# Kernel tuning notes

Measured on AMD Instinct MI355X. Metric: run time of the kernel, lower is better.

## Reference

```python
import jax, jax.numpy as jnp
import numpy as np

N_NODES = 50000
N_EDGES = 800000
D_IN = 64
D_OUT = 64


def setup_inputs() -> dict:
    key = jax.random.key(0)
    k1, k2, k3, k4 = jax.random.split(key, 4)
    x = jax.random.normal(k1, (N_NODES, D_IN), dtype=jnp.float32)
    src = jax.random.randint(k2, (N_EDGES,), 0, N_NODES, dtype=jnp.int64)
    dst = jax.random.randint(k3, (N_EDGES,), 0, N_NODES, dtype=jnp.int64)
    W = jax.random.normal(k4, (D_IN, D_OUT), dtype=jnp.float32) / np.sqrt(D_IN)
    b = jnp.zeros((D_OUT,), dtype=jnp.float32)
    return {"x": x, "src": src, "dst": dst, "W": W, "b": b}


def reference(x, src, dst, W, b):
    # DGL GraphConv, norm='both': out = D_in^{-1/2} A D_out^{-1/2} x W + b
    n = x.shape[0]
    ones = jnp.ones(src.shape[0], dtype=x.dtype)
    out_deg = jax.ops.segment_sum(ones, src, num_segments=n)  # out-degree of each node
    in_deg = jax.ops.segment_sum(ones, dst, num_segments=n)   # in-degree of each node
    norm_src = jax.lax.rsqrt(jnp.clip(out_deg, 1.0))          # [N]
    norm_dst = jax.lax.rsqrt(jnp.clip(in_deg, 1.0))           # [N]
    h = x * norm_src[:, None]                                 # [N, D_in]
    msg = jnp.take(h, src, axis=0)                            # [E, D_in] gather
    agg = jax.ops.segment_sum(msg, dst, num_segments=n)       # [N, D_in] scatter-add
    agg = agg * norm_dst[:, None]
    return agg @ W + b                                        # [N, D_out]
```

## Files before the change

### kernel.cpp

```cpp
#include <hip/hip_runtime.h>
#include <hip/hip_fp16.h>

#define N_NODES 50000
#define N_EDGES 800000
#define D 64

#define SLICES 80
#define I4S (N_EDGES / 4 / SLICES)
#define NWORDS 12512

#define CTR_OFF    0
#define BASE_OFF   64
#define END_OFF    200064
#define SNORM_OFF  400064
#define DNORM_OFF  600064
#define INW_OFF    800064
#define OUTW_OFF   850112
#define SSRC_OFF   900160
#define PART_OFF   4100160
#define Y16_OFF    PART_OFF
#define ZERO_BYTES 64

__global__ __launch_bounds__(256) void degree_lds_kernel(const int4* __restrict__ src4,
                                                         const int4* __restrict__ dst4,
                                                         unsigned int* __restrict__ partial) {
    __shared__ unsigned int hist[NWORDS];
    int tid = threadIdx.x;
    for (int i = tid; i < NWORDS; i += 256) hist[i] = 0;
    __syncthreads();

    int role  = blockIdx.x & 1;
    int slice = blockIdx.x >> 1;
    const int4* e = role ? dst4 : src4;
    int beg = slice * I4S, end = beg + I4S;
    for (int i = beg + tid; i < end; i += 256) {
        int4 v = e[i];
        atomicAdd(&hist[v.x >> 2], 1u << ((v.x & 3) * 8));
        atomicAdd(&hist[v.y >> 2], 1u << ((v.y & 3) * 8));
        atomicAdd(&hist[v.z >> 2], 1u << ((v.z & 3) * 8));
        atomicAdd(&hist[v.w >> 2], 1u << ((v.w & 3) * 8));
    }
    __syncthreads();

    unsigned int* p = partial + (size_t)blockIdx.x * NWORDS;
    for (int i = tid; i < NWORDS; i += 256) p[i] = hist[i];
}

__global__ __launch_bounds__(256) void merge_kernel(unsigned int* __restrict__ partial,
                                                    unsigned int* __restrict__ INW,
                                                    unsigned int* __restrict__ OUTW) {
    int w = blockIdx.x * blockDim.x + threadIdx.x;
    if (w >= 12500) return;
    unsigned int accin = 0, accout = 0;
#pragma unroll 4
    for (int s = 0; s < SLICES; s++) {
        size_t od = (size_t)(2 * s) * NWORDS + w;
        size_t dd = (size_t)(2 * s + 1) * NWORDS + w;
        accout += partial[od];
        unsigned int v = partial[dd];
        partial[dd] = accin;
        accin += v;
    }
    INW[w] = accin;
    OUTW[w] = accout;
}

__global__ __launch_bounds__(256) void scan_kernel(const unsigned int* __restrict__ INW,
                                                   const unsigned int* __restrict__ OUTW,
                                                   int* __restrict__ base,
                                                   int* __restrict__ rend,
                                                   float* __restrict__ snorm,
                                                   float* __restrict__ dnorm,
                                                   int* __restrict__ ctr) {
    int n = blockIdx.x * blockDim.x + threadIdx.x;
    int lane = threadIdx.x & 63;
    int din = 0, dout = 0;
    if (n < N_NODES) {
        int sh = (n & 3) * 8;
        din  = (INW[n >> 2] >> sh) & 0xFF;
        dout = (OUTW[n >> 2] >> sh) & 0xFF;
    }
    int sum = din;
#pragma unroll
    for (int off = 1; off < 64; off <<= 1) {
        int v = __shfl_up(sum, off);
        if (lane >= off) sum += v;
    }
    int wtot = __shfl(sum, 63);
    int wbase = 0;
    if (lane == 63) wbase = atomicAdd(ctr, wtot);
    wbase = __shfl(wbase, 63);
    if (n < N_NODES) {
        int myb = wbase + (sum - din);
        base[n] = myb;
        rend[n] = myb + din;
        dnorm[n] = rsqrtf(fmaxf((float)din, 1.0f));
        snorm[n] = rsqrtf(fmaxf((float)dout, 1.0f));
    }
}

__global__ __launch_bounds__(256) void fill_kernel(const int4* __restrict__ src4,
                                                   const int4* __restrict__ dst4,
                                                   const unsigned int* __restrict__ partial,
                                                   const int* __restrict__ base,
                                                   int* __restrict__ ssrc) {
    __shared__ unsigned int hist[NWORDS];
    int tid = threadIdx.x;
    for (int i = tid; i < NWORDS; i += 256) hist[i] = 0;
    __syncthreads();

    int s = blockIdx.x;
    const int4* sp = src4 + (size_t)s * I4S;
    const int4* dp = dst4 + (size_t)s * I4S;
    const unsigned int* pref = partial + (size_t)(2 * s + 1) * NWORDS;

    for (int i = tid; i < I4S; i += 256) {
        int4 sv = sp[i], tv = dp[i];
#define FILL_ONE(T, S)                                                        \
        {                                                                     \
            int t = (T); int sh = (t & 3) * 8;                                \
            unsigned int old = atomicAdd(&hist[t >> 2], 1u << sh);            \
            int local = (old >> sh) & 0xFF;                                   \
            int p = base[t] + (int)((pref[t >> 2] >> sh) & 0xFFu) + local;    \
            ssrc[p] = (S);                                                    \
        }
        FILL_ONE(tv.x, sv.x)
        FILL_ONE(tv.y, sv.y)
        FILL_ONE(tv.z, sv.z)
        FILL_ONE(tv.w, sv.w)
#undef FILL_ONE
    }
}

#define YBLK 1024
__global__ __launch_bounds__(256, 4) void y_kernel(const float* __restrict__ x,
                                                   const float* __restrict__ snorm,
                                                   const float* __restrict__ W,
                                                   __half* __restrict__ y16) {
    int lane = threadIdx.x & 63;
    int wave = (blockIdx.x << 2) | (threadIdx.x >> 6);

    float Wreg[D];
#pragma unroll
    for (int k = 0; k < D; k++) Wreg[k] = W[k * D + lane];

    for (int n = wave; n < N_NODES; n += YBLK * 4) {
        float hv = x[(size_t)n * D + lane] * snorm[n];
        int hb = __float_as_int(hv);
        float p0 = 0.f, p1 = 0.f, p2 = 0.f, p3 = 0.f;
#pragma unroll
        for (int k = 0; k < D; k += 4) {
            p0 = fmaf(__int_as_float(__builtin_amdgcn_readlane(hb, k + 0)), Wreg[k + 0], p0);
            p1 = fmaf(__int_as_float(__builtin_amdgcn_readlane(hb, k + 1)), Wreg[k + 1], p1);
            p2 = fmaf(__int_as_float(__builtin_amdgcn_readlane(hb, k + 2)), Wreg[k + 2], p2);
            p3 = fmaf(__int_as_float(__builtin_amdgcn_readlane(hb, k + 3)), Wreg[k + 3], p3);
        }
        y16[(size_t)n * D + lane] = __float2half((p0 + p1) + (p2 + p3));
    }
}

#define GBLK 2048
__global__ __launch_bounds__(256, 8) void gather_kernel(const __half* __restrict__ y16,
                                                        const int* __restrict__ ssrc,
                                                        const int* __restrict__ base,
                                                        const int* __restrict__ rend,
                                                        const float* __restrict__ dnorm,
                                                        const float* __restrict__ b,
                                                        float* __restrict__ out) {
    int lane = threadIdx.x & 63;
    int wave = (blockIdx.x << 2) | (threadIdx.x >> 6);
    float breg = b[lane];
    const __half* yl = y16 + lane;

    for (int n = wave; n < N_NODES; n += GBLK * 4) {
        int beg = base[n];
        int end = rend[n];
        float a0 = 0.f, a1 = 0.f, a2 = 0.f, a3 = 0.f;
        float a4 = 0.f, a5 = 0.f, a6 = 0.f, a7 = 0.f;
        int i = beg;
        for (; i + 8 <= end; i += 8) {
            int s0 = ssrc[i],     s1 = ssrc[i + 1], s2 = ssrc[i + 2], s3 = ssrc[i + 3];
            int s4 = ssrc[i + 4], s5 = ssrc[i + 5], s6 = ssrc[i + 6], s7 = ssrc[i + 7];
            a0 += __half2float(yl[(size_t)s0 * D]);
            a1 += __half2float(yl[(size_t)s1 * D]);
            a2 += __half2float(yl[(size_t)s2 * D]);
            a3 += __half2float(yl[(size_t)s3 * D]);
            a4 += __half2float(yl[(size_t)s4 * D]);
            a5 += __half2float(yl[(size_t)s5 * D]);
            a6 += __half2float(yl[(size_t)s6 * D]);
            a7 += __half2float(yl[(size_t)s7 * D]);
        }
        for (; i + 4 <= end; i += 4) {
            int s0 = ssrc[i], s1 = ssrc[i + 1], s2 = ssrc[i + 2], s3 = ssrc[i + 3];
            a0 += __half2float(yl[(size_t)s0 * D]);
            a1 += __half2float(yl[(size_t)s1 * D]);
            a2 += __half2float(yl[(size_t)s2 * D]);
            a3 += __half2float(yl[(size_t)s3 * D]);
        }
        for (; i < end; ++i) {
            a0 += __half2float(yl[(size_t)ssrc[i] * D]);
        }
        float acc = ((a0 + a4) + (a1 + a5)) + ((a2 + a6) + (a3 + a7));
        out[(size_t)n * D + lane] = fmaf(acc, dnorm[n], breg);
    }
}

extern "C" void kernel_launch(void* const* d_in, const int* in_sizes, int n_in,
                              void* d_out, int out_size, void* d_ws, size_t ws_size,
                              hipStream_t stream) {
    const float* x   = (const float*)d_in[0];
    const int*   src = (const int*)d_in[1];
    const int*   dst = (const int*)d_in[2];
    const float* W   = (const float*)d_in[3];
    const float* b   = (const float*)d_in[4];
    float* out = (float*)d_out;

    char* ws = (char*)d_ws;
    int*          ctr   = (int*)(ws + CTR_OFF);
    int*          base  = (int*)(ws + BASE_OFF);
    int*          rend  = (int*)(ws + END_OFF);
    float*        snorm = (float*)(ws + SNORM_OFF);
    float*        dnorm = (float*)(ws + DNORM_OFF);
    unsigned int* INW   = (unsigned int*)(ws + INW_OFF);
    unsigned int* OUTW  = (unsigned int*)(ws + OUTW_OFF);
    int*          ssrc  = (int*)(ws + SSRC_OFF);
    unsigned int* part  = (unsigned int*)(ws + PART_OFF);
    __half*       y16   = (__half*)(ws + Y16_OFF);

    hipMemsetAsync(d_ws, 0, ZERO_BYTES, stream);

    degree_lds_kernel<<<2 * SLICES, 256, 0, stream>>>((const int4*)src,
                                                      (const int4*)dst, part);
    merge_kernel<<<(12500 + 255) / 256, 256, 0, stream>>>(part, INW, OUTW);
    scan_kernel<<<(N_NODES + 255) / 256, 256, 0, stream>>>(INW, OUTW, base, rend,
                                                           snorm, dnorm, ctr);
    fill_kernel<<<SLICES, 256, 0, stream>>>((const int4*)src, (const int4*)dst,
                                            part, base, ssrc);
    y_kernel<<<YBLK, 256, 0, stream>>>(x, snorm, W, y16);
    gather_kernel<<<GBLK, 256, 0, stream>>>(y16, ssrc, base, rend, dnorm, b, out);
}
```

Measured before the change: 171.7 us.

## Fuse merge and scan kernels, drop memset, vectorize LDS init and half2 gather

Merges the degree merge and scan kernels into one that scans four packed node degrees per thread and writes int4/float4 outputs. Removes the memset by zeroing the counter inside the degree kernel, and vectorizes the LDS clear and copy-out with uint4. Rewrites the gather so each lane loads a half2 and the two halves of a lane pair take alternate edges, combined with a shuffle and written with nontemporal stores. Together these cut launch count and per-edge load instructions, at the cost of more complex indexing and a cross-lane reduction.

```diff
diff --git a/kernel.cpp b/kernel.cpp
--- a/kernel.cpp
+++ b/kernel.cpp
@@ -9,24 +9,26 @@
 #define I4S (N_EDGES / 4 / SLICES)
 #define NWORDS 12512
 
+typedef float vfloat2 __attribute__((ext_vector_type(2)));
+
 #define CTR_OFF    0
-#define BASE_OFF   64
-#define END_OFF    200064
-#define SNORM_OFF  400064
-#define DNORM_OFF  600064
-#define INW_OFF    800064
-#define OUTW_OFF   850112
-#define SSRC_OFF   900160
-#define PART_OFF   4100160
+#define BASE_OFF   256
+#define END_OFF    200320
+#define SNORM_OFF  400384
+#define DNORM_OFF  600448
+#define SSRC_OFF   800512
+#define PART_OFF   4000768
 #define Y16_OFF    PART_OFF
-#define ZERO_BYTES 64
 
 __global__ __launch_bounds__(256) void degree_lds_kernel(const int4* __restrict__ src4,
                                                          const int4* __restrict__ dst4,
-                                                         unsigned int* __restrict__ partial) {
+                                                         unsigned int* __restrict__ partial,
+                                                         int* __restrict__ ctr) {
     __shared__ unsigned int hist[NWORDS];
     int tid = threadIdx.x;
-    for (int i = tid; i < NWORDS; i += 256) hist[i] = 0;
+    if (blockIdx.x == 0 && tid == 0) *ctr = 0;
+    uint4* h4 = (uint4*)hist;
+    for (int i = tid; i < NWORDS / 4; i += 256) h4[i] = make_uint4(0, 0, 0, 0);
     __syncthreads();
 
     int role  = blockIdx.x & 1;
@@ -42,60 +44,59 @@
     }
     __syncthreads();
 
-    unsigned int* p = partial + (size_t)blockIdx.x * NWORDS;
-    for (int i = tid; i < NWORDS; i += 256) p[i] = hist[i];
-}
-
-__global__ __launch_bounds__(256) void merge_kernel(unsigned int* __restrict__ partial,
-                                                    unsigned int* __restrict__ INW,
-                                                    unsigned int* __restrict__ OUTW) {
+    uint4* p4 = (uint4*)(partial + (size_t)blockIdx.x * NWORDS);
+    for (int i = tid; i < NWORDS / 4; i += 256) p4[i] = h4[i];
+}
+
+__global__ __launch_bounds__(256) void merge_scan_kernel(unsigned int* __restrict__ partial,
+                                                         int* __restrict__ base,
+                                                         int* __restrict__ rend,
+                                                         float* __restrict__ snorm,
+                                                         float* __restrict__ dnorm,
+                                                         int* __restrict__ ctr) {
     int w = blockIdx.x * blockDim.x + threadIdx.x;
-    if (w >= 12500) return;
+    int lane = threadIdx.x & 63;
     unsigned int accin = 0, accout = 0;
+    if (w < 12500) {
+        unsigned int* po = partial + w;
+        unsigned int* pd = partial + NWORDS + w;
 #pragma unroll 4
-    for (int s = 0; s < SLICES; s++) {
-        size_t od = (size_t)(2 * s) * NWORDS + w;
-        size_t dd = (size_t)(2 * s + 1) * NWORDS + w;
-        accout += partial[od];
-        unsigned int v = partial[dd];
-        partial[dd] = accin;
-        accin += v;
-    }
-    INW[w] = accin;
-    OUTW[w] = accout;
-}
-
-__global__ __launch_bounds__(256) void scan_kernel(const unsigned int* __restrict__ INW,
-                                                   const unsigned int* __restrict__ OUTW,
-                                                   int* __restrict__ base,
-                                                   int* __restrict__ rend,
-                                                   float* __restrict__ snorm,
-                                                   float* __restrict__ dnorm,
-                                                   int* __restrict__ ctr) {
-    int n = blockIdx.x * blockDim.x + threadIdx.x;
-    int lane = threadIdx.x & 63;
-    int din = 0, dout = 0;
-    if (n < N_NODES) {
-        int sh = (n & 3) * 8;
-        din  = (INW[n >> 2] >> sh) & 0xFF;
-        dout = (OUTW[n >> 2] >> sh) & 0xFF;
-    }
-    int sum = din;
+        for (int s = 0; s < SLICES; s++) {
+            size_t off = (size_t)(2 * s) * NWORDS;
+            accout += po[off];
+            unsigned int v = pd[off];
+            pd[off] = accin;
+            accin += v;
+        }
+    }
+    int d0 = accin & 0xFF, d1 = (accin >> 8) & 0xFF,
+        d2 = (accin >> 16) & 0xFF, d3 = (accin >> 24) & 0xFF;
+    int tsum = d0 + d1 + d2 + d3;
+    int run = tsum;
 #pragma unroll
     for (int off = 1; off < 64; off <<= 1) {
-        int v = __shfl_up(sum, off);
-        if (lane >= off) sum += v;
-    }
-    int wtot = __shfl(sum, 63);
+        int v = __shfl_up(run, off);
+        if (lane >= off) run += v;
+    }
+    int wtot = __shfl(run, 63);
     int wbase = 0;
     if (lane == 63) wbase = atomicAdd(ctr, wtot);
     wbase = __shfl(wbase, 63);
-    if (n < N_NODES) {
-        int myb = wbase + (sum - din);
-        base[n] = myb;
-        rend[n] = myb + din;
-        dnorm[n] = rsqrtf(fmaxf((float)din, 1.0f));
-        snorm[n] = rsqrtf(fmaxf((float)dout, 1.0f));
+    if (w < 12500) {
+        int b0 = wbase + run - tsum;
+        int b1 = b0 + d0, b2 = b1 + d1, b3 = b2 + d2;
+        ((int4*)base)[w] = make_int4(b0, b1, b2, b3);
+        ((int4*)rend)[w] = make_int4(b1, b2, b3, b3 + d3);
+        ((float4*)dnorm)[w] = make_float4(rsqrtf(fmaxf((float)d0, 1.f)),
+                                          rsqrtf(fmaxf((float)d1, 1.f)),
+                                          rsqrtf(fmaxf((float)d2, 1.f)),
+                                          rsqrtf(fmaxf((float)d3, 1.f)));
+        int o0 = accout & 0xFF, o1 = (accout >> 8) & 0xFF,
+            o2 = (accout >> 16) & 0xFF, o3 = (accout >> 24) & 0xFF;
+        ((float4*)snorm)[w] = make_float4(rsqrtf(fmaxf((float)o0, 1.f)),
+                                          rsqrtf(fmaxf((float)o1, 1.f)),
+                                          rsqrtf(fmaxf((float)o2, 1.f)),
+                                          rsqrtf(fmaxf((float)o3, 1.f)));
     }
 }
 
@@ -106,7 +107,8 @@
                                                    int* __restrict__ ssrc) {
     __shared__ unsigned int hist[NWORDS];
     int tid = threadIdx.x;
-    for (int i = tid; i < NWORDS; i += 256) hist[i] = 0;
+    uint4* h4 = (uint4*)hist;
+    for (int i = tid; i < NWORDS / 4; i += 256) h4[i] = make_uint4(0, 0, 0, 0);
     __syncthreads();
 
     int s = blockIdx.x;
@@ -160,7 +162,7 @@
 }
 
 #define GBLK 2048
-__global__ __launch_bounds__(256, 8) void gather_kernel(const __half* __restrict__ y16,
+__global__ __launch_bounds__(256, 8) void gather_kernel(const __half2* __restrict__ y2,
                                                         const int* __restrict__ ssrc,
                                                         const int* __restrict__ base,
                                                         const int* __restrict__ rend,
@@ -168,40 +170,58 @@
                                                         const float* __restrict__ b,
                                                         float* __restrict__ out) {
     int lane = threadIdx.x & 63;
+    int half = lane & 1;
+    int col  = lane >> 1;
     int wave = (blockIdx.x << 2) | (threadIdx.x >> 6);
-    float breg = b[lane];
-    const __half* yl = y16 + lane;
+
+    float2 b2 = ((const float2*)b)[col];
+    const __half2* yl = y2 + col;
 
     for (int n = wave; n < N_NODES; n += GBLK * 4) {
-        int beg = base[n];
-        int end = rend[n];
-        float a0 = 0.f, a1 = 0.f, a2 = 0.f, a3 = 0.f;
-        float a4 = 0.f, a5 = 0.f, a6 = 0.f, a7 = 0.f;
-        int i = beg;
-        for (; i + 8 <= end; i += 8) {
-            int s0 = ssrc[i],     s1 = ssrc[i + 1], s2 = ssrc[i + 2], s3 = ssrc[i + 3];
-            int s4 = ssrc[i + 4], s5 = ssrc[i + 5], s6 = ssrc[i + 6], s7 = ssrc[i + 7];
-            a0 += __half2float(yl[(size_t)s0 * D]);
-            a1 += __half2float(yl[(size_t)s1 * D]);
-            a2 += __half2float(yl[(size_t)s2 * D]);
-            a3 += __half2float(yl[(size_t)s3 * D]);
-            a4 += __half2float(yl[(size_t)s4 * D]);
-            a5 += __half2float(yl[(size_t)s5 * D]);
-            a6 += __half2float(yl[(size_t)s6 * D]);
-            a7 += __half2float(yl[(size_t)s7 * D]);
-        }
-        for (; i + 4 <= end; i += 4) {
-            int s0 = ssrc[i], s1 = ssrc[i + 1], s2 = ssrc[i + 2], s3 = ssrc[i + 3];
-            a0 += __half2float(yl[(size_t)s0 * D]);
-            a1 += __half2float(yl[(size_t)s1 * D]);
-            a2 += __half2float(yl[(size_t)s2 * D]);
-            a3 += __half2float(yl[(size_t)s3 * D]);
-        }
-        for (; i < end; ++i) {
-            a0 += __half2float(yl[(size_t)ssrc[i] * D]);
-        }
-        float acc = ((a0 + a4) + (a1 + a5)) + ((a2 + a6) + (a3 + a7));
-        out[(size_t)n * D + lane] = fmaf(acc, dnorm[n], breg);
+        int beg = base[n], end = rend[n];
+        float ax0 = 0.f, ay0 = 0.f, ax1 = 0.f, ay1 = 0.f;
+        float ax2 = 0.f, ay2 = 0.f, ax3 = 0.f, ay3 = 0.f;
+        float ax4 = 0.f, ay4 = 0.f, ax5 = 0.f, ay5 = 0.f;
+        float ax6 = 0.f, ay6 = 0.f, ax7 = 0.f, ay7 = 0.f;
+        int i0 = beg;
+        for (; i0 + 16 <= end; i0 += 16) {
+            int e = i0 + half;
+            int s0 = ssrc[e],      s1 = ssrc[e + 2],  s2 = ssrc[e + 4],  s3 = ssrc[e + 6];
+            int s4 = ssrc[e + 8],  s5 = ssrc[e + 10], s6 = ssrc[e + 12], s7 = ssrc[e + 14];
+            float2 f0 = __half22float2(yl[(size_t)s0 * 32]);
+            float2 f1 = __half22float2(yl[(size_t)s1 * 32]);
+            float2 f2 = __half22float2(yl[(size_t)s2 * 32]);
+            float2 f3 = __half22float2(yl[(size_t)s3 * 32]);
+            float2 f4 = __half22float2(yl[(size_t)s4 * 32]);
+            float2 f5 = __half22float2(yl[(size_t)s5 * 32]);
+            float2 f6 = __half22float2(yl[(size_t)s6 * 32]);
+            float2 f7 = __half22float2(yl[(size_t)s7 * 32]);
+            ax0 += f0.x; ay0 += f0.y; ax1 += f1.x; ay1 += f1.y;
+            ax2 += f2.x; ay2 += f2.y; ax3 += f3.x; ay3 += f3.y;
+            ax4 += f4.x; ay4 += f4.y; ax5 += f5.x; ay5 += f5.y;
+            ax6 += f6.x; ay6 += f6.y; ax7 += f7.x; ay7 += f7.y;
+        }
+        for (; i0 + 2 <= end; i0 += 2) {
+            int s = ssrc[i0 + half];
+            float2 f = __half22float2(yl[(size_t)s * 32]);
+            ax0 += f.x; ay0 += f.y;
+        }
+        if (i0 < end && half == 0) {
+            int s = ssrc[i0];
+            float2 f = __half22float2(yl[(size_t)s * 32]);
+            ax1 += f.x; ay1 += f.y;
+        }
+        float sx = ((ax0 + ax1) + (ax2 + ax3)) + ((ax4 + ax5) + (ax6 + ax7));
+        float sy = ((ay0 + ay1) + (ay2 + ay3)) + ((ay4 + ay5) + (ay6 + ay7));
+        sx += __shfl(sx, lane ^ 1);
+        sy += __shfl(sy, lane ^ 1);
+        if (half == 0) {
+            float dn = dnorm[n];
+            vfloat2 o;
+            o.x = fmaf(sx, dn, b2.x);
+            o.y = fmaf(sy, dn, b2.y);
+            __builtin_nontemporal_store(o, (vfloat2*)(out + (size_t)n * D) + col);
+        }
     }
 }
 
@@ -221,21 +241,17 @@
     int*          rend  = (int*)(ws + END_OFF);
     float*        snorm = (float*)(ws + SNORM_OFF);
     float*        dnorm = (float*)(ws + DNORM_OFF);
-    unsigned int* INW   = (unsigned int*)(ws + INW_OFF);
-    unsigned int* OUTW  = (unsigned int*)(ws + OUTW_OFF);
     int*          ssrc  = (int*)(ws + SSRC_OFF);
     unsigned int* part  = (unsigned int*)(ws + PART_OFF);
     __half*       y16   = (__half*)(ws + Y16_OFF);
 
-    hipMemsetAsync(d_ws, 0, ZERO_BYTES, stream);
-
     degree_lds_kernel<<<2 * SLICES, 256, 0, stream>>>((const int4*)src,
-                                                      (const int4*)dst, part);
-    merge_kernel<<<(12500 + 255) / 256, 256, 0, stream>>>(part, INW, OUTW);
-    scan_kernel<<<(N_NODES + 255) / 256, 256, 0, stream>>>(INW, OUTW, base, rend,
-                                                           snorm, dnorm, ctr);
+                                                      (const int4*)dst, part, ctr);
+    merge_scan_kernel<<<(12500 + 255) / 256, 256, 0, stream>>>(part, base, rend,
+                                                               snorm, dnorm, ctr);
     fill_kernel<<<SLICES, 256, 0, stream>>>((const int4*)src, (const int4*)dst,
                                             part, base, ssrc);
     y_kernel<<<YBLK, 256, 0, stream>>>(x, snorm, W, y16);
-    gather_kernel<<<GBLK, 256, 0, stream>>>(y16, ssrc, base, rend, dnorm, b, out);
-}
+    gather_kernel<<<GBLK, 256, 0, stream>>>((const __half2*)y16, ssrc, base, rend,
+                                            dnorm, b, out);
+}
```

Result: faster. 161.9 us (-5.7%).
